# Kernel optimization log

Hardware: AMD Instinct MI355X
Metric: run time of the kernel (lower is better)

Reference implementation:

```python
import jax, jax.numpy as jnp
import numpy as np

EPS = 1e-5

def layer_norm(x, g, b):
    mu = jnp.mean(x, axis=-1, keepdims=True)
    var = jnp.mean((x - mu) ** 2, axis=-1, keepdims=True)
    return (x - mu) * jax.lax.rsqrt(var + EPS) * g + b

def setup_inputs() -> dict:
    key = jax.random.key(0)
    ks = jax.random.split(key, 13)
    B, N, C, H = 2, 2048, 1024, 16
    Dff = 4 * C
    s = lambda k, shape, fan_in: jax.random.normal(k, shape, jnp.float32) * (1.0 / np.sqrt(fan_in))
    return {
        "x": jax.random.normal(ks[0], (B, N, C), jnp.float32),
        "ln1_g": jnp.ones((C,), jnp.float32),
        "ln1_b": jnp.zeros((C,), jnp.float32),
        "qkv_w": s(ks[1], (3 * C, C), C),
        "qkv_b": jnp.zeros((3 * C,), jnp.float32),
        "proj_w": s(ks[2], (C, C), C),
        "proj_b": jnp.zeros((C,), jnp.float32),
        "ln2_g": jnp.ones((C,), jnp.float32),
        "ln2_b": jnp.zeros((C,), jnp.float32),
        "fc1_w": s(ks[3], (Dff, C), C),
        "fc1_b": jnp.zeros((Dff,), jnp.float32),
        "fc2_w": s(ks[4], (C, Dff), Dff),
        "fc2_b": jnp.zeros((C,), jnp.float32),
    }

def reference(x, ln1_g, ln1_b, qkv_w, qkv_b, proj_w, proj_b, ln2_g, ln2_b, fc1_w, fc1_b, fc2_w, fc2_b):
    B, N, C = x.shape
    H = 16
    D = C // H
    # --- attention sub-block (pre-norm) ---
    h = layer_norm(x, ln1_g, ln1_b)
    qkv = h @ qkv_w.T + qkv_b                      # [B,N,3C]
    qkv = qkv.reshape(B, N, 3, H, D).transpose(2, 0, 3, 1, 4)  # [3,B,H,N,D]
    q, k, v = qkv[0], qkv[1], qkv[2]
    attn = jnp.einsum('bhnd,bhmd->bhnm', q, k) * (D ** -0.5)   # [B,H,N,N]
    attn = jax.nn.softmax(attn, axis=-1)
    o = jnp.einsum('bhnm,bhmd->bhnd', attn, v)     # [B,H,N,D]
    o = o.transpose(0, 2, 1, 3).reshape(B, N, C)
    x = x + (o @ proj_w.T + proj_b)
    # --- MLP sub-block (pre-norm) ---
    h = layer_norm(x, ln2_g, ln2_b)
    h = jax.nn.gelu(h @ fc1_w.T + fc1_b, approximate=False)
    x = x + (h @ fc2_w.T + fc2_b)
    return x
```

## Files before the change

kernel.cpp:

```cpp
#include <hip/hip_runtime.h>
#include <hip/hip_bf16.h>
#include <math.h>

typedef __bf16 bf16;
typedef __bf16 bf16x8 __attribute__((ext_vector_type(8)));
typedef __bf16 bf16x4 __attribute__((ext_vector_type(4)));
typedef float  f32x4  __attribute__((ext_vector_type(4)));
typedef float  f32x16 __attribute__((ext_vector_type(16)));
typedef int    i32x4  __attribute__((ext_vector_type(4)));

typedef __attribute__((address_space(1))) void gvoid;
typedef __attribute__((address_space(3))) void lvoid;
#define GLOAD_LDS16(gp, lp) __builtin_amdgcn_global_load_lds((gvoid*)(gp), (lvoid*)(lp), 16, 0, 0)

typedef __attribute__((address_space(3))) bf16x8 as3_bf16x8;
typedef __attribute__((address_space(3))) bf16   as3_bf16;
__device__ __forceinline__ bf16x8 lds_rd8(const void* p) {
  return *(const as3_bf16x8*)p;
}
__device__ __forceinline__ void lds_wr8(void* p, bf16x8 v) {
  *(as3_bf16x8*)p = v;
}
__device__ __forceinline__ void lds_wr1(void* p, bf16 v) {
  *(as3_bf16*)p = v;
}

__global__ __launch_bounds__(256) void prep(
    const float* __restrict__ qkvw, const float* __restrict__ projw,
    const float* __restrict__ fc1w, const float* __restrict__ fc2w,
    bf16* __restrict__ qkvw_h, bf16* __restrict__ projw_h,
    bf16* __restrict__ fc1w_h, bf16* __restrict__ fc2w_h,
    const float* __restrict__ x, const float* __restrict__ g,
    const float* __restrict__ b, bf16* __restrict__ h1) {
  int blk = blockIdx.x;
  if (blk < 12288) {
    const float* in; bf16* out; int base;
    if (blk < 3072)      { in = qkvw; out = qkvw_h; base = blk; }
    else if (blk < 4096) { in = projw; out = projw_h; base = blk - 3072; }
    else if (blk < 8192) { in = fc1w; out = fc1w_h; base = blk - 4096; }
    else                 { in = fc2w; out = fc2w_h; base = blk - 8192; }
    int i = (base * 256 + threadIdx.x) * 4;
    f32x4 v = *(const f32x4*)(in + i);
    bf16x4 o;
    #pragma unroll
    for (int e = 0; e < 4; ++e) o[e] = (bf16)v[e];
    *(bf16x4*)(out + i) = o;
    return;
  }
  int w = threadIdx.x >> 6, l = threadIdx.x & 63;
  size_t row = (size_t)(blk - 12288) * 4 + w;
  const float* xr = x + row * 1024;
  float f[16];
  #pragma unroll
  for (int c = 0; c < 4; ++c) {
    f32x4 v = *(const f32x4*)(xr + c * 256 + l * 4);
    #pragma unroll
    for (int e = 0; e < 4; ++e) f[c * 4 + e] = v[e];
  }
  float s = 0.f, ss = 0.f;
  #pragma unroll
  for (int e = 0; e < 16; ++e) { s += f[e]; ss += f[e] * f[e]; }
  #pragma unroll
  for (int d = 1; d < 64; d <<= 1) { s += __shfl_xor(s, d); ss += __shfl_xor(ss, d); }
  float mean = s * (1.f / 1024.f);
  float var  = ss * (1.f / 1024.f) - mean * mean;
  float rstd = rsqrtf(var + 1e-5f);
  #pragma unroll
  for (int c = 0; c < 4; ++c) {
    f32x4 gv = *(const f32x4*)(g + c * 256 + l * 4);
    f32x4 bv = *(const f32x4*)(b + c * 256 + l * 4);
    bf16x4 ov;
    #pragma unroll
    for (int e = 0; e < 4; ++e)
      ov[e] = (bf16)((f[c * 4 + e] - mean) * rstd * gv[e] + bv[e]);
    *(bf16x4*)(h1 + row * 1024 + c * 256 + l * 4) = ov;
  }
}

__global__ __launch_bounds__(256) void ln_f32(const float* __restrict__ x,
    const float* __restrict__ g, const float* __restrict__ b, bf16* __restrict__ out) {
  int w = threadIdx.x >> 6, l = threadIdx.x & 63;
  size_t row = (size_t)blockIdx.x * 4 + w;
  const float* xr = x + row * 1024;
  float f[16];
  #pragma unroll
  for (int c = 0; c < 4; ++c) {
    f32x4 v = *(const f32x4*)(xr + c * 256 + l * 4);
    #pragma unroll
    for (int e = 0; e < 4; ++e) f[c * 4 + e] = v[e];
  }
  float s = 0.f, ss = 0.f;
  #pragma unroll
  for (int e = 0; e < 16; ++e) { s += f[e]; ss += f[e] * f[e]; }
  #pragma unroll
  for (int d = 1; d < 64; d <<= 1) { s += __shfl_xor(s, d); ss += __shfl_xor(ss, d); }
  float mean = s * (1.f / 1024.f);
  float var  = ss * (1.f / 1024.f) - mean * mean;
  float rstd = rsqrtf(var + 1e-5f);
  #pragma unroll
  for (int c = 0; c < 4; ++c) {
    f32x4 gv = *(const f32x4*)(g + c * 256 + l * 4);
    f32x4 bv = *(const f32x4*)(b + c * 256 + l * 4);
    bf16x4 ov;
    #pragma unroll
    for (int e = 0; e < 4; ++e)
      ov[e] = (bf16)((f[c * 4 + e] - mean) * rstd * gv[e] + bv[e]);
    *(bf16x4*)(out + row * 1024 + c * 256 + l * 4) = ov;
  }
}

#define SWZ(tp) ((tp) ^ ((((tp) >> 9) & 1) << 5))
#define STAGE(buf, op, half, kt_) do { \
    const char* gp_ = (const char*)((op) ? Wp : Ap); \
    int t0_ = (op) ? colBase : rowBase; \
    const int P_ = (op) ? 12 : 13; \
    _Pragma("unroll") for (int s_ = 0; s_ < 2; ++s_) { \
      int b14_ = w * 2048 + s_ * 1024; \
      int tb_ = ((b14_ >> P_) << (P_ + 1)) | ((half) << P_) | (b14_ & ((1 << P_) - 1)); \
      int tq_ = SWZ(tb_ + l * 16); \
      GLOAD_LDS16(gp_ + ((size_t)(t0_ + (tq_ >> 7)) * lda + (size_t)(kt_) * 64) * 2 + (tq_ & 127), \
                  smbase + (buf) * 65536 + (op) * 32768 + tb_); \
    } \
  } while (0)
#define LDA(buf, mi, kk) lds_rd8(smbase + (buf) * 65536 + \
    SWZ((wm * 128 + (mi) * 16 + lr) * 128 + (kk) * 64 + lg * 16))
#define LDB(buf, ni, kk) lds_rd8(smbase + (buf) * 65536 + 32768 + \
    SWZ((wn * 64 + (ni) * 16 + lr) * 128 + (kk) * 64 + lg * 16))
#define RD_A(buf, MI0) { _Pragma("unroll") for (int i_ = 0; i_ < 4; ++i_) \
    _Pragma("unroll") for (int k_ = 0; k_ < 2; ++k_) a[i_][k_] = LDA(buf, (MI0) + i_, k_); }
#define RD_B(buf, NI0) { _Pragma("unroll") for (int j_ = 0; j_ < 2; ++j_) \
    _Pragma("unroll") for (int k_ = 0; k_ < 2; ++k_) bq[(NI0) + j_][k_] = LDB(buf, (NI0) + j_, k_); }
#define MFMA16(MI0, NI0) do { __builtin_amdgcn_s_setprio(1); \
    _Pragma("unroll") for (int i_ = 0; i_ < 4; ++i_) \
    _Pragma("unroll") for (int j_ = 0; j_ < 2; ++j_) \
    _Pragma("unroll") for (int k_ = 0; k_ < 2; ++k_) \
      acc[(MI0) + i_][(NI0) + j_] = __builtin_amdgcn_mfma_f32_16x16x32_bf16( \
          a[i_][k_], bq[(NI0) + j_][k_], acc[(MI0) + i_][(NI0) + j_], 0, 0, 0); \
    __builtin_amdgcn_s_setprio(0); } while (0)
#define BARX() __builtin_amdgcn_s_barrier()
#define LGK0() asm volatile("s_waitcnt lgkmcnt(0)")
#define VM4()  asm volatile("s_waitcnt vmcnt(4)")

template<int ACT, int HASBIAS, typename TO>
__global__ __launch_bounds__(512, 1) void gemm256(const bf16* __restrict__ Ap,
    const bf16* __restrict__ Wp, const float* __restrict__ bias,
    TO* __restrict__ out, int lda, int N, int klen, int nbx, size_t outSlice) {
  __shared__ bf16 smem_[2][2][256 * 64];
  char* smbase = (char*)smem_;
  int tid = threadIdx.x, w = tid >> 6, l = tid & 63, lr = l & 15, lg = l >> 4;
  int wm = w >> 2, wn = w & 3;
  int q = gridDim.x >> 3;
  int wg = ((int)blockIdx.x & 7) * q + ((int)blockIdx.x >> 3);
  int rowBase = (wg / nbx) * 256, colBase = (wg % nbx) * 256;
  Ap += (size_t)blockIdx.y * klen;
  Wp += (size_t)blockIdx.y * klen;
  out += (size_t)blockIdx.y * outSlice;

  f32x4 acc[8][4];
  const f32x4 fz = {0.f, 0.f, 0.f, 0.f};
  #pragma unroll
  for (int i = 0; i < 8; ++i)
    #pragma unroll
    for (int j = 0; j < 4; ++j) acc[i][j] = fz;
  bf16x8 a[4][2], bq[4][2];
  int nkt = klen >> 6;

  STAGE(0, 1, 0, 0); STAGE(0, 1, 1, 0); STAGE(0, 0, 0, 0); STAGE(0, 0, 1, 0);
  STAGE(1, 1, 0, 1); STAGE(1, 1, 1, 1);
  VM4(); BARX();

  for (int t = 0; t < nkt; t += 2) {
    int t1 = t + 1;
    int t2 = t + 2 < nkt ? t + 2 : nkt - 1;
    int t3 = t + 3 < nkt ? t + 3 : nkt - 1;
    RD_A(0, 0); RD_B(0, 0);
    STAGE(1, 0, 0, t1);
    BARX(); LGK0(); MFMA16(0, 0); BARX();
    RD_B(0, 2);
    STAGE(1, 0, 1, t1);
    BARX(); LGK0(); MFMA16(0, 2); BARX();
    RD_A(0, 4);
    STAGE(0, 1, 0, t2);
    BARX(); LGK0(); MFMA16(4, 0); BARX();
    STAGE(0, 1, 1, t2);
    VM4();
    BARX(); MFMA16(4, 2); BARX();
    RD_A(1, 0); RD_B(1, 0);
    STAGE(0, 0, 0, t2);
    BARX(); LGK0(); MFMA16(0, 0); BARX();
    RD_B(1, 2);
    STAGE(0, 0, 1, t2);
    BARX(); LGK0(); MFMA16(0, 2); BARX();
    RD_A(1, 4);
    STAGE(1, 1, 0, t3);
    BARX(); LGK0(); MFMA16(4, 0); BARX();
    STAGE(1, 1, 1, t3);
    VM4();
    BARX(); MFMA16(4, 2); BARX();
  }

  #pragma unroll
  for (int ni = 0; ni < 4; ++ni) {
    int col = colBase + wn * 64 + ni * 16 + lr;
    float bv = HASBIAS ? bias[col] : 0.f;
    #pragma unroll
    for (int mi = 0; mi < 8; ++mi) {
      #pragma unroll
      for (int jj = 0; jj < 4; ++jj) {
        int row2 = rowBase + wm * 128 + mi * 16 + lg * 4 + jj;
        float v = acc[mi][ni][jj] + bv;
        if constexpr (ACT == 1) v = 0.5f * v * (1.f + erff(v * 0.70710678118f));
        out[(size_t)row2 * N + col] = (TO)v;
      }
    }
  }
}

__global__ __launch_bounds__(256) void projred_ln(const bf16* __restrict__ part,
    const float* __restrict__ x, const float* __restrict__ pb,
    const float* __restrict__ g, const float* __restrict__ bb,
    float* __restrict__ x1, bf16* __restrict__ h2) {
  int w = threadIdx.x >> 6, l = threadIdx.x & 63;
  size_t row = (size_t)blockIdx.x * 4 + w;
  size_t rb = row * 1024;
  float f[16];
  #pragma unroll
  for (int c = 0; c < 4; ++c) {
    int off = c * 256 + l * 4;
    f32x4 v = *(const f32x4*)(x + rb + off);
    v += *(const f32x4*)(pb + off);
    #pragma unroll
    for (int sl = 0; sl < 4; ++sl) {
      bf16x4 pv = *(const bf16x4*)(part + (size_t)sl * 4194304 + rb + off);
      #pragma unroll
      for (int e = 0; e < 4; ++e) v[e] += (float)pv[e];
    }
    *(f32x4*)(x1 + rb + off) = v;
    #pragma unroll
    for (int e = 0; e < 4; ++e) f[c * 4 + e] = v[e];
  }
  float s = 0.f, ss = 0.f;
  #pragma unroll
  for (int e = 0; e < 16; ++e) { s += f[e]; ss += f[e] * f[e]; }
  #pragma unroll
  for (int d = 1; d < 64; d <<= 1) { s += __shfl_xor(s, d); ss += __shfl_xor(ss, d); }
  float mean = s * (1.f / 1024.f);
  float var  = ss * (1.f / 1024.f) - mean * mean;
  float rstd = rsqrtf(var + 1e-5f);
  #pragma unroll
  for (int c = 0; c < 4; ++c) {
    int off = c * 256 + l * 4;
    f32x4 gv = *(const f32x4*)(g + off);
    f32x4 bv = *(const f32x4*)(bb + off);
    bf16x4 ov;
    #pragma unroll
    for (int e = 0; e < 4; ++e)
      ov[e] = (bf16)((f[c * 4 + e] - mean) * rstd * gv[e] + bv[e]);
    *(bf16x4*)(h2 + rb + off) = ov;
  }
}

__global__ __launch_bounds__(256) void fc2_red(const bf16* __restrict__ part,
    const float* __restrict__ x1, const float* __restrict__ bias,
    float* __restrict__ out) {
  int i = (blockIdx.x * 256 + threadIdx.x) * 4;
  f32x4 s = *(const f32x4*)(x1 + i);
  s += *(const f32x4*)(bias + (i & 1023));
  #pragma unroll
  for (int k = 0; k < 4; ++k) {
    bf16x4 pv = *(const bf16x4*)(part + (size_t)k * 4194304 + i);
    #pragma unroll
    for (int e = 0; e < 4; ++e) s[e] += (float)pv[e];
  }
  *(f32x4*)(out + i) = s;
}

template<int ACT, int HASRES, typename TO>
__global__ __launch_bounds__(256) void gemm_bt(const bf16* __restrict__ A,
    const bf16* __restrict__ W, const float* __restrict__ bias,
    const float* __restrict__ res, TO* __restrict__ out, int M, int N, int K) {
  __shared__ bf16 As[128 * 32];
  __shared__ bf16 Bs[128 * 32];
  int tid = threadIdx.x;
  int w = tid >> 6, l = tid & 63;
  int lr = l & 15, lg = l >> 4;
  int wm = w >> 1, wn = w & 1;
  int rowBase = blockIdx.y * 128;
  int colBase = blockIdx.x * 128;
  f32x4 acc[4][4];
  const f32x4 fz = {0.f, 0.f, 0.f, 0.f};
  #pragma unroll
  for (int i = 0; i < 4; ++i)
    #pragma unroll
    for (int j = 0; j < 4; ++j) acc[i][j] = fz;
  for (int kt = 0; kt < K; kt += 32) {
    __syncthreads();
    #pragma unroll
    for (int j = 0; j < 2; ++j) {
      int u = (w * 2 + j) * 64 + l;
      int r = u >> 2, cb = (u & 3) * 8;
      GLOAD_LDS16(A + (size_t)(rowBase + r) * K + kt + cb, As + (w * 2 + j) * 512);
      GLOAD_LDS16(W + (size_t)(colBase + r) * K + kt + cb, Bs + (w * 2 + j) * 512);
    }
    __syncthreads();
    bf16x8 af[4], bfr[4];
    #pragma unroll
    for (int mi = 0; mi < 4; ++mi)
      af[mi] = lds_rd8(As + (wm * 64 + mi * 16 + lr) * 32 + lg * 8);
    #pragma unroll
    for (int ni = 0; ni < 4; ++ni)
      bfr[ni] = lds_rd8(Bs + (wn * 64 + ni * 16 + lr) * 32 + lg * 8);
    #pragma unroll
    for (int mi = 0; mi < 4; ++mi)
      #pragma unroll
      for (int ni = 0; ni < 4; ++ni)
        acc[mi][ni] = __builtin_amdgcn_mfma_f32_16x16x32_bf16(af[mi], bfr[ni], acc[mi][ni], 0, 0, 0);
  }
  #pragma unroll
  for (int ni = 0; ni < 4; ++ni) {
    int col = colBase + wn * 64 + ni * 16 + lr;
    float bv = bias[col];
    #pragma unroll
    for (int mi = 0; mi < 4; ++mi) {
      #pragma unroll
      for (int jj = 0; jj < 4; ++jj) {
        int row2 = rowBase + wm * 64 + mi * 16 + lg * 4 + jj;
        float v = acc[mi][ni][jj] + bv;
        if constexpr (ACT == 1) v = 0.5f * v * (1.f + erff(v * 0.70710678118f));
        if constexpr (HASRES)   v += res[(size_t)row2 * N + col];
        out[(size_t)row2 * N + col] = (TO)v;
      }
    }
  }
}

#define MKFRAG(S, T, OUT) do { \
    int a_, b_, c_, d_; \
    asm("v_cvt_pk_bf16_f32 %0, %1, %2" : "=v"(a_) : "v"((S)[8*(T)+0]), "v"((S)[8*(T)+1])); \
    asm("v_cvt_pk_bf16_f32 %0, %1, %2" : "=v"(b_) : "v"((S)[8*(T)+4]), "v"((S)[8*(T)+5])); \
    asm("v_cvt_pk_bf16_f32 %0, %1, %2" : "=v"(c_) : "v"((S)[8*(T)+2]), "v"((S)[8*(T)+3])); \
    asm("v_cvt_pk_bf16_f32 %0, %1, %2" : "=v"(d_) : "v"((S)[8*(T)+6]), "v"((S)[8*(T)+7])); \
    asm("v_permlane32_swap_b32 %0, %1" : "+v"(a_), "+v"(b_)); \
    asm("v_permlane32_swap_b32 %0, %1" : "+v"(c_), "+v"(d_)); \
    i32x4 wv_ = {a_, c_, b_, d_}; \
    OUT = __builtin_bit_cast(bf16x8, wv_); \
  } while (0)

#define ATILE(BO, DOLOAD, DOSTAGE) do { \
    if (DOLOAD) { \
      kg0 = *(const bf16x8*)kp0; kp0 += step; \
      kg1 = *(const bf16x8*)kp1; kp1 += step; \
      vg0 = *(const bf16x8*)vp0; \
      vg1 = *(const bf16x8*)(vp0 + 32); vp0 += step; \
    } \
    bf16x8 ka[2][4]; \
    _Pragma("unroll") for (int kb = 0; kb < 2; ++kb) \
      _Pragma("unroll") for (int dk = 0; dk < 4; ++dk) \
        ka[kb][dk] = lds_rd8(abase + (BO) + kb * 4096 + doff[dk]); \
    f32x16 sc0 = zz, sc1 = zz; \
    __builtin_amdgcn_s_setprio(1); \
    _Pragma("unroll") for (int dk = 0; dk < 4; ++dk) { \
      sc0 = __builtin_amdgcn_mfma_f32_32x32x16_bf16(ka[0][dk], qf[dk], sc0, 0, 0, 0); \
      sc1 = __builtin_amdgcn_mfma_f32_32x32x16_bf16(ka[1][dk], qf[dk], sc1, 0, 0, 0); \
    } \
    __builtin_amdgcn_s_setprio(0); \
    _Pragma("unroll") for (int r = 0; r < 16; ++r) sc0[r] = exp2f(sc0[r]); \
    _Pragma("unroll") for (int r = 0; r < 16; ++r) sc1[r] = exp2f(sc1[r]); \
    { \
      float t0_ = (sc0[0] + sc0[1]) + (sc0[2] + sc0[3]); \
      float t1_ = (sc0[4] + sc0[5]) + (sc0[6] + sc0[7]); \
      float t2_ = (sc0[8] + sc0[9]) + (sc0[10] + sc0[11]); \
      float t3_ = (sc0[12] + sc0[13]) + (sc0[14] + sc0[15]); \
      float t4_ = (sc1[0] + sc1[1]) + (sc1[2] + sc1[3]); \
      float t5_ = (sc1[4] + sc1[5]) + (sc1[6] + sc1[7]); \
      float t6_ = (sc1[8] + sc1[9]) + (sc1[10] + sc1[11]); \
      float t7_ = (sc1[12] + sc1[13]) + (sc1[14] + sc1[15]); \
      float rs = ((t0_ + t1_) + (t2_ + t3_)) + ((t4_ + t5_) + (t6_ + t7_)); \
      rs += __shfl_xor(rs, 32); \
      srow += rs; \
    } \
    bf16x8 pa0, pa1, pa2, pa3; \
    MKFRAG(sc0, 0, pa0); MKFRAG(sc0, 1, pa1); \
    MKFRAG(sc1, 0, pa2); MKFRAG(sc1, 1, pa3); \
    bf16x8 vb[2][4]; \
    _Pragma("unroll") for (int db = 0; db < 2; ++db) \
      _Pragma("unroll") for (int ks = 0; ks < 4; ++ks) \
        vb[db][ks] = lds_rd8(vbase + (BO) + db * 4096 + doff[ks]); \
    __builtin_amdgcn_s_setprio(1); \
    oa0 = __builtin_amdgcn_mfma_f32_32x32x16_bf16(pa0, vb[0][0], oa0, 0, 0, 0); \
    oa0 = __builtin_amdgcn_mfma_f32_32x32x16_bf16(pa1, vb[0][1], oa0, 0, 0, 0); \
    oa0 = __builtin_amdgcn_mfma_f32_32x32x16_bf16(pa2, vb[0][2], oa0, 0, 0, 0); \
    oa0 = __builtin_amdgcn_mfma_f32_32x32x16_bf16(pa3, vb[0][3], oa0, 0, 0, 0); \
    oa1 = __builtin_amdgcn_mfma_f32_32x32x16_bf16(pa0, vb[1][0], oa1, 0, 0, 0); \
    oa1 = __builtin_amdgcn_mfma_f32_32x32x16_bf16(pa1, vb[1][1], oa1, 0, 0, 0); \
    oa1 = __builtin_amdgcn_mfma_f32_32x32x16_bf16(pa2, vb[1][2], oa1, 0, 0, 0); \
    oa1 = __builtin_amdgcn_mfma_f32_32x32x16_bf16(pa3, vb[1][3], oa1, 0, 0, 0); \
    __builtin_amdgcn_s_setprio(0); \
    if (DOSTAGE) { \
      lds_wr8(ksw + ((BO) ^ 8192), kg0); \
      lds_wr8(ksw + 4096 + ((BO) ^ 8192), kg1); \
      _Pragma("unroll") for (int e = 0; e < 8; ++e) { \
        lds_wr1(vtw + ((BO) ^ 8192) + e * 128 + (l2 ^ (e << 4)), vg0[e]); \
        lds_wr1(vtw + ((BO) ^ 8192) + 4096 + e * 128 + (l2 ^ (e << 4)), vg1[e]); \
      } \
      __syncthreads(); \
    } \
  } while (0)

__global__ __launch_bounds__(256) void attn_kernel(const bf16* __restrict__ qkv,
                                                   bf16* __restrict__ o) {
  const int Nn = 2048, C3 = 3072;
  int tid = threadIdx.x, w = tid >> 6, l = tid & 63;
  int q32 = l & 31, hi = l >> 5, hi4 = hi * 4;
  int lin = blockIdx.x;
  int wg = (lin & 7) * 64 + (lin >> 3);
  int qb = wg & 15, bh = wg >> 4;
  int b = bh >> 4, h = bh & 15;
  size_t hb = (size_t)b * Nn * C3 + h * 64;
  const bf16* Qp = qkv + hb;
  __shared__ bf16 Ks[2][64 * 64];
  __shared__ bf16 Vt[2][64 * 64];

  int q0w = qb * 128 + w * 32;
  bf16x8 qf[4];
  {
    const bf16* qrow = Qp + (size_t)(q0w + q32) * C3 + 8 * hi;
    #pragma unroll
    for (int dk = 0; dk < 4; ++dk) {
      bf16x8 t = *(const bf16x8*)(qrow + 16 * dk);
      #pragma unroll
      for (int e = 0; e < 8; ++e) qf[dk][e] = (bf16)((float)t[e] * 0.18033688f);
    }
  }

  int swz = (l & 7) << 4;
  int kr0 = tid >> 3, c80 = (tid & 7) * 8;
  char* ksw = (char*)Ks + kr0 * 128 + ((c80 * 2) ^ ((kr0 & 7) << 4));
  char* vtw = (char*)Vt + w * 1024;
  int l2 = l * 2;
  const char* abase = (const char*)Ks + q32 * 128;
  const char* vbase = (const char*)Vt + q32 * 128;
  int doff[4];
  #pragma unroll
  for (int dk = 0; dk < 4; ++dk) doff[dk] = (32 * dk + 16 * hi) ^ swz;

  const bf16* kp0 = qkv + hb + 1024 + (size_t)kr0 * C3 + c80;
  const bf16* kp1 = kp0 + (size_t)32 * C3;
  const bf16* vp0 = qkv + hb + 2048 + (size_t)l * C3 + w * 8;
  const int step = 64 * C3;

  f32x16 zz;
  #pragma unroll
  for (int i = 0; i < 16; ++i) zz[i] = 0.f;
  f32x16 oa0 = zz, oa1 = zz;
  float srow = 0.f;

  bf16x8 kg0 = *(const bf16x8*)kp0; kp0 += step;
  bf16x8 kg1 = *(const bf16x8*)kp1; kp1 += step;
  bf16x8 vg0 = *(const bf16x8*)vp0;
  bf16x8 vg1 = *(const bf16x8*)(vp0 + 32); vp0 += step;
  lds_wr8(ksw, kg0);
  lds_wr8(ksw + 4096, kg1);
  #pragma unroll
  for (int e = 0; e < 8; ++e) {
    lds_wr1(vtw + e * 128 + (l2 ^ (e << 4)), vg0[e]);
    lds_wr1(vtw + 4096 + e * 128 + (l2 ^ (e << 4)), vg1[e]);
  }
  __syncthreads();

  for (int tt = 0; tt < 16; ++tt) {
    ATILE(0,    true,     true);
    ATILE(8192, tt < 15,  tt < 15);
  }

  float inv = 1.f / srow;
  bf16* ob = o + ((size_t)b * Nn + q0w + hi4) * 1024 + h * 64 + q32;
  #pragma unroll
  for (int r = 0; r < 16; ++r) {
    const int cr = (r & 3) + 8 * (r >> 2);
    float invr = __shfl(inv, cr + hi4);
    ob[(size_t)cr * 1024]      = (bf16)(oa0[r] * invr);
    ob[(size_t)cr * 1024 + 32] = (bf16)(oa1[r] * invr);
  }
}

extern "C" void kernel_launch(void* const* d_in, const int* in_sizes, int n_in,
                              void* d_out, int out_size, void* d_ws, size_t ws_size,
                              hipStream_t stream) {
  (void)in_sizes; (void)n_in; (void)out_size;
  const float* x     = (const float*)d_in[0];
  const float* ln1g  = (const float*)d_in[1];
  const float* ln1b  = (const float*)d_in[2];
  const float* qkvw  = (const float*)d_in[3];
  const float* qkvb  = (const float*)d_in[4];
  const float* projw = (const float*)d_in[5];
  const float* projb = (const float*)d_in[6];
  const float* ln2g  = (const float*)d_in[7];
  const float* ln2b  = (const float*)d_in[8];
  const float* fc1w  = (const float*)d_in[9];
  const float* fc1b  = (const float*)d_in[10];
  const float* fc2w  = (const float*)d_in[11];
  const float* fc2b  = (const float*)d_in[12];

  char* ws = (char*)d_ws;
  bf16*  qkvw_h = (bf16*)(ws);
  bf16*  projw_h= (bf16*)(ws + (6ull  << 20));
  bf16*  fc1w_h = (bf16*)(ws + (8ull  << 20));
  bf16*  fc2w_h = (bf16*)(ws + (16ull << 20));
  bf16*  h1     = (bf16*)(ws + (24ull << 20));
  bf16*  qkv    = (bf16*)(ws + (32ull << 20));
  bf16*  ov     = (bf16*)(ws + (64ull << 20));
  float* x1     = (float*)(ws + (72ull << 20));
  bf16*  parts  = (bf16*)(ws + (96ull << 20));
  bf16*  h2  = h1;
  bf16*  ffn = qkv;
  bool big = ws_size >= (160ull << 20);

  const int M = 4096;
  prep<<<dim3(12288 + 1024), 256, 0, stream>>>(qkvw, projw, fc1w, fc2w,
      qkvw_h, projw_h, fc1w_h, fc2w_h, x, ln1g, ln1b, h1);
  gemm256<0, 1, bf16><<<dim3(192), dim3(512), 0, stream>>>(
      h1, qkvw_h, qkvb, qkv, 1024, 3072, 1024, 12, 0);
  attn_kernel<<<dim3(512), 256, 0, stream>>>(qkv, ov);
  if (big) {
    gemm256<0, 0, bf16><<<dim3(64, 4), dim3(512), 0, stream>>>(
        ov, projw_h, nullptr, parts, 1024, 1024, 256, 4, 4194304ull);
    projred_ln<<<dim3(1024), 256, 0, stream>>>(parts, x, projb, ln2g, ln2b, x1, h2);
  } else {
    gemm_bt<0, 1, float><<<dim3(8, 32), 256, 0, stream>>>(
        ov, projw_h, projb, x, x1, M, 1024, 1024);
    ln_f32<<<dim3(1024), 256, 0, stream>>>(x1, ln2g, ln2b, h2);
  }
  gemm256<1, 1, bf16><<<dim3(256), dim3(512), 0, stream>>>(
      h2, fc1w_h, fc1b, ffn, 1024, 4096, 1024, 16, 0);
  if (big) {
    gemm256<0, 0, bf16><<<dim3(64, 4), dim3(512), 0, stream>>>(
        ffn, fc2w_h, nullptr, parts, 4096, 1024, 1024, 4, 4194304ull);
    fc2_red<<<dim3(4096), 256, 0, stream>>>(parts, x1, fc2b, (float*)d_out);
  } else {
    gemm_bt<0, 1, float><<<dim3(8, 32), 256, 0, stream>>>(
        ffn, fc2w_h, fc2b, x1, (float*)d_out, M, 1024, 4096);
  }
}
```

Before: 278.9 us.

## Simplify GEMM main loop to whole-tile double buffering with one barrier

Replaces the fine-grained 8-phase pipeline, which issued half-tile async loads between MFMA groups with many barriers and partial vmcnt waits, with a simple double-buffered loop. Each iteration issues a full next-tile prefetch, computes the whole current tile, then waits for all loads and syncs once. This cuts barrier count and scheduling complexity but reduces overlap granularity, since vmcnt(0) waits on the whole prefetch each tile.

```diff
diff --git a/kernel.cpp b/kernel.cpp
--- a/kernel.cpp
+++ b/kernel.cpp
@@ -121,6 +121,10 @@
       GLOAD_LDS16(gp_ + ((size_t)(t0_ + (tq_ >> 7)) * lda + (size_t)(kt_) * 64) * 2 + (tq_ & 127), \
                   smbase + (buf) * 65536 + (op) * 32768 + tb_); \
     } \
+  } while (0)
+#define STAGEFULL(buf, kt_) do { \
+    STAGE(buf, 0, 0, kt_); STAGE(buf, 0, 1, kt_); \
+    STAGE(buf, 1, 0, kt_); STAGE(buf, 1, 1, kt_); \
   } while (0)
 #define LDA(buf, mi, kk) lds_rd8(smbase + (buf) * 65536 + \
     SWZ((wm * 128 + (mi) * 16 + lr) * 128 + (kk) * 64 + lg * 16))
@@ -139,7 +143,16 @@
     __builtin_amdgcn_s_setprio(0); } while (0)
 #define BARX() __builtin_amdgcn_s_barrier()
 #define LGK0() asm volatile("s_waitcnt lgkmcnt(0)")
-#define VM4()  asm volatile("s_waitcnt vmcnt(4)")
+#define VM0()  asm volatile("s_waitcnt vmcnt(0)")
+
+#define GTILE(CUR, NXT, tn, DOSTAGE) do { \
+    if (DOSTAGE) { STAGEFULL(NXT, tn); } \
+    RD_A(CUR, 0); RD_B(CUR, 0); RD_B(CUR, 2); \
+    LGK0(); MFMA16(0, 0); MFMA16(0, 2); \
+    RD_A(CUR, 4); \
+    LGK0(); MFMA16(4, 0); MFMA16(4, 2); \
+    VM0(); BARX(); \
+  } while (0)
 
 template<int ACT, int HASBIAS, typename TO>
 __global__ __launch_bounds__(512, 1) void gemm256(const bf16* __restrict__ Ap,
@@ -165,38 +178,12 @@
   bf16x8 a[4][2], bq[4][2];
   int nkt = klen >> 6;
 
-  STAGE(0, 1, 0, 0); STAGE(0, 1, 1, 0); STAGE(0, 0, 0, 0); STAGE(0, 0, 1, 0);
-  STAGE(1, 1, 0, 1); STAGE(1, 1, 1, 1);
-  VM4(); BARX();
+  STAGEFULL(0, 0);
+  VM0(); BARX();
 
   for (int t = 0; t < nkt; t += 2) {
-    int t1 = t + 1;
-    int t2 = t + 2 < nkt ? t + 2 : nkt - 1;
-    int t3 = t + 3 < nkt ? t + 3 : nkt - 1;
-    RD_A(0, 0); RD_B(0, 0);
-    STAGE(1, 0, 0, t1);
-    BARX(); LGK0(); MFMA16(0, 0); BARX();
-    RD_B(0, 2);
-    STAGE(1, 0, 1, t1);
-    BARX(); LGK0(); MFMA16(0, 2); BARX();
-    RD_A(0, 4);
-    STAGE(0, 1, 0, t2);
-    BARX(); LGK0(); MFMA16(4, 0); BARX();
-    STAGE(0, 1, 1, t2);
-    VM4();
-    BARX(); MFMA16(4, 2); BARX();
-    RD_A(1, 0); RD_B(1, 0);
-    STAGE(0, 0, 0, t2);
-    BARX(); LGK0(); MFMA16(0, 0); BARX();
-    RD_B(1, 2);
-    STAGE(0, 0, 1, t2);
-    BARX(); LGK0(); MFMA16(0, 2); BARX();
-    RD_A(1, 4);
-    STAGE(1, 1, 0, t3);
-    BARX(); LGK0(); MFMA16(4, 0); BARX();
-    STAGE(1, 1, 1, t3);
-    VM4();
-    BARX(); MFMA16(4, 2); BARX();
+    GTILE(0, 1, t + 1, true);
+    GTILE(1, 0, t + 2, (t + 2 < nkt));
   }
 
   #pragma unroll
```

Result: faster. 256.8 us (-7.9%).
